# Kernel tuning notes

Hardware: AMD Instinct MI355X
Metric: run time of the kernel (lower is better)

The kernel has to match this reference:

```python
import jax, jax.numpy as jnp
import numpy as np

NUM_HEADS = 8
CH_PER_HEAD = 40
NORM_GROUPS = 32
EPS = 1e-5


def setup_inputs() -> dict:
    key = jax.random.key(0)
    ks = jax.random.split(key, 8)
    B, C, H, W = 2, 320, 48, 48
    hid = NUM_HEADS * CH_PER_HEAD  # 320
    w_std = 0.02
    return {
        "x": jax.random.normal(ks[0], (B, C, H, W), dtype=jnp.float32),
        "gamma": jnp.ones((C,), dtype=jnp.float32),
        "beta": jnp.zeros((C,), dtype=jnp.float32),
        "Wq": jax.random.normal(ks[1], (hid, C), dtype=jnp.float32) * w_std,
        "bq": jax.random.normal(ks[2], (hid,), dtype=jnp.float32) * w_std,
        "Wk": jax.random.normal(ks[3], (hid, C), dtype=jnp.float32) * w_std,
        "bk": jax.random.normal(ks[4], (hid,), dtype=jnp.float32) * w_std,
        "Wv": jax.random.normal(ks[5], (hid, C), dtype=jnp.float32) * w_std,
        "bv": jax.random.normal(ks[6], (hid,), dtype=jnp.float32) * w_std,
        "Wo": jax.random.normal(ks[7], (C, hid), dtype=jnp.float32) * w_std,
        "bo": jnp.zeros((C,), dtype=jnp.float32),
    }


def _group_norm(x, gamma, beta):
    # x: [B, C, H, W]; GroupNorm over (C//G, H, W) per group, affine per-channel.
    B, C, H, W = x.shape
    xg = x.reshape(B, NORM_GROUPS, C // NORM_GROUPS, H, W)
    mean = xg.mean(axis=(2, 3, 4), keepdims=True)
    var = xg.var(axis=(2, 3, 4), keepdims=True)
    xn = ((xg - mean) * jax.lax.rsqrt(var + EPS)).reshape(B, C, H, W)
    return xn * gamma[None, :, None, None] + beta[None, :, None, None]


def reference(x, gamma, beta, Wq, bq, Wk, bk, Wv, bv, Wo, bo):
    B, C, H, W = x.shape
    N = H * W
    h, d = NUM_HEADS, CH_PER_HEAD
    scale = d ** (-0.25)  # applied to both q and k (net 1/sqrt(d))

    xn = _group_norm(x, gamma, beta).reshape(B, C, N)  # embedding = x_n (self-attn)

    # 1x1 Conv1d == matmul over channel dim
    q = jnp.einsum('oc,bcn->bon', Wq, xn) + bq[None, :, None]
    k = jnp.einsum('oc,bcn->bon', Wk, xn) + bk[None, :, None]
    v = jnp.einsum('oc,bcn->bon', Wv, xn) + bv[None, :, None]

    # b (h d) n -> b h d n
    q = q.reshape(B, h, d, N)
    k = k.reshape(B, h, d, N)
    v = v.reshape(B, h, d, N)

    attn = jax.nn.softmax(
        jnp.einsum('bhdi,bhdj->bhij', q * scale, k * scale), axis=-1
    )  # [B, h, N, N]
    out = jnp.einsum('bhij,bhdj->bhdi', attn, v).reshape(B, h * d, N)

    out = jnp.einsum('oc,bcn->bon', Wo, out) + bo[None, :, None]
    out = out.reshape(B, C, H, W)
    return x + out  # shapes match -> residual
```

## Files before the change

kernel.cpp:

```cpp
#include <hip/hip_runtime.h>
#include <hip/hip_bf16.h>

#define C_DIM   320
#define N_SP    2304
#define NHEADS  8
#define DHEAD   40
#define GROUPS  32
#define CPG     10
#define BATCH   2
#define DPAD    64
#define VPAD    48
#define W_ELEMS (C_DIM * C_DIM)
#define NSPLIT  4
#define TILES_PER_SPLIT 9
#define PSLOTS  41

typedef __bf16 bf16x8 __attribute__((ext_vector_type(8)));
typedef __bf16 bf16x4 __attribute__((ext_vector_type(4)));
typedef __bf16 bf16x2 __attribute__((ext_vector_type(2)));
typedef float  f32x4  __attribute__((ext_vector_type(4)));

typedef const __attribute__((address_space(1))) void* gas_ptr;
typedef __attribute__((address_space(3))) void* las_ptr;

#define MFMA16(a, b, c) __builtin_amdgcn_mfma_f32_16x16x32_bf16((a), (b), (c), 0, 0, 0)

__device__ __forceinline__ void stage8(const char* gbase, char* lbase,
                                       int chunk, int lane)
{
    const int row = chunk * 8 + (lane >> 3);
    const int cs  = (lane & 7) * 16;
    __builtin_amdgcn_global_load_lds(
        (gas_ptr)(gbase + (size_t)row * (C_DIM * 2) + (cs ^ ((row & 7) << 4))),
        (las_ptr)(lbase + chunk * 1024 + lane * 16), 16, 0, 0);
}

__device__ __forceinline__ bf16x8 lds_frag(const char* lbase, int row, int cbyte)
{
    return *(const bf16x8*)(lbase + row * 128 + (cbyte ^ ((row & 7) << 4)));
}

__global__ __launch_bounds__(256) void prep_kernel(
    const float* __restrict__ x, float* __restrict__ partials,
    const float* __restrict__ Wq, const float* __restrict__ Wk,
    const float* __restrict__ Wv, const float* __restrict__ Wo,
    __bf16* __restrict__ Wqb, __bf16* __restrict__ Wkb,
    __bf16* __restrict__ Wvb, __bf16* __restrict__ Wob,
    __bf16* __restrict__ Qt, __bf16* __restrict__ Kt, __bf16* __restrict__ Vb)
{
    if (blockIdx.x < 512) {
        const int bid = blockIdx.x;
        const int bg = bid >> 3, p = bid & 7;
        const int b = bg >> 5, g = bg & 31;
        const float* xp = x + ((size_t)b * C_DIM + g * CPG) * N_SP + p * 288;
        const int tid = threadIdx.x;

        float sum = 0.f, sq = 0.f;
        #pragma unroll
        for (int c = 0; c < CPG; ++c) {
            for (int nl = tid; nl < 288; nl += 256) {
                const float v = xp[(size_t)c * N_SP + nl];
                sum += v; sq += v * v;
            }
        }
        #pragma unroll
        for (int off = 32; off; off >>= 1) {
            sum += __shfl_xor(sum, off);
            sq  += __shfl_xor(sq, off);
        }
        __shared__ float red[2][4];
        if ((tid & 63) == 0) { red[0][tid >> 6] = sum; red[1][tid >> 6] = sq; }
        __syncthreads();
        if (tid == 0) {
            partials[2 * bid]     = red[0][0] + red[0][1] + red[0][2] + red[0][3];
            partials[2 * bid + 1] = red[1][0] + red[1][1] + red[1][2] + red[1][3];
        }
    } else if (blockIdx.x < 612) {
        const int i = ((blockIdx.x - 512) * 256 + threadIdx.x) * 4;
        f32x4 a;
        bf16x4 o;
        a = *(const f32x4*)(Wq + i);
        #pragma unroll
        for (int e = 0; e < 4; ++e) o[e] = (__bf16)a[e];
        *(bf16x4*)(Wqb + i) = o;
        a = *(const f32x4*)(Wk + i);
        #pragma unroll
        for (int e = 0; e < 4; ++e) o[e] = (__bf16)a[e];
        *(bf16x4*)(Wkb + i) = o;
        a = *(const f32x4*)(Wv + i);
        #pragma unroll
        for (int e = 0; e < 4; ++e) o[e] = (__bf16)a[e];
        *(bf16x4*)(Wvb + i) = o;
        a = *(const f32x4*)(Wo + i);
        #pragma unroll
        for (int e = 0; e < 4; ++e) o[e] = (__bf16)a[e];
        *(bf16x4*)(Wob + i) = o;
    } else {
        const int t = (blockIdx.x - 612) * 256 + threadIdx.x;
        const bf16x8 z = {};
        __bf16* q = Qt + (size_t)t * DPAD + 40;
        __bf16* k = Kt + (size_t)t * DPAD + 40;
        *(bf16x8*)(q) = z; *(bf16x8*)(q + 8) = z; *(bf16x8*)(q + 16) = z;
        *(bf16x8*)(k) = z; *(bf16x8*)(k + 8) = z; *(bf16x8*)(k + 16) = z;
        const int bh = t / N_SP;
        const int rem = t - bh * N_SP;
        const int r = rem / 288, n8 = rem - r * 288;
        bf16x8 v = z;
        if (r == 0) {
            #pragma unroll
            for (int e = 0; e < 8; ++e) v[e] = (__bf16)1.0f;
        }
        *(bf16x8*)(Vb + ((size_t)bh * VPAD + 40 + r) * N_SP + n8 * 8) = v;
    }
}

__global__ __launch_bounds__(256) void gn_apply(
    const float* __restrict__ x,
    const float* __restrict__ gamma, const float* __restrict__ beta,
    const float* __restrict__ partials, __bf16* __restrict__ xn_t)
{
    const int bid = blockIdx.x;
    const int bg = bid >> 3, p = bid & 7;
    const int b = bg >> 5, g = bg & 31;
    const int c0 = g * CPG;

    float sum = 0.f, sq = 0.f;
    #pragma unroll
    for (int i = 0; i < 8; ++i) {
        sum += partials[(bg * 8 + i) * 2];
        sq  += partials[(bg * 8 + i) * 2 + 1];
    }
    const float inv_n = 1.0f / (float)(CPG * N_SP);
    const float mean = sum * inv_n;
    const float rstd = rsqrtf(sq * inv_n - mean * mean + 1e-5f);

    float ga[CPG], be[CPG];
    #pragma unroll
    for (int c = 0; c < CPG; ++c) {
        ga[c] = gamma[c0 + c] * rstd;
        be[c] = beta[c0 + c] - mean * ga[c];
    }

    const float* xp = x + ((size_t)b * C_DIM + c0) * N_SP + p * 288;
    for (int nl = threadIdx.x; nl < 288; nl += 256) {
        const int n = p * 288 + nl;
        __bf16* dst = xn_t + ((size_t)b * N_SP + n) * C_DIM + c0;
        #pragma unroll
        for (int j = 0; j < CPG / 2; ++j) {
            const float v0 = xp[(size_t)(2 * j) * N_SP + nl]     * ga[2 * j]     + be[2 * j];
            const float v1 = xp[(size_t)(2 * j + 1) * N_SP + nl] * ga[2 * j + 1] + be[2 * j + 1];
            bf16x2 t; t[0] = (__bf16)v0; t[1] = (__bf16)v1;
            *(bf16x2*)(dst + 2 * j) = t;
        }
    }
}

__global__ __launch_bounds__(256) void gemm_qkv(
    const __bf16* __restrict__ Wqb, const __bf16* __restrict__ Wkb, const __bf16* __restrict__ Wvb,
    const float* __restrict__ bq, const float* __restrict__ bk, const float* __restrict__ bv,
    const __bf16* __restrict__ Xt,
    __bf16* __restrict__ Qt, __bf16* __restrict__ Kt, __bf16* __restrict__ Vb)
{
    __shared__ __align__(16) char Ws[2][64 * 128];
    __shared__ __align__(16) char Xs[2][64 * 128];

    const int z = blockIdx.z;
    const int b = z / 3;
    const int which = z - 3 * b;
    const __bf16* W   = (which == 0) ? Wqb : (which == 1) ? Wkb : Wvb;
    const float* bias = (which == 0) ? bq : (which == 1) ? bk : bv;
    const float scale = (which == 0) ? 0.15811388300841897f
                      : (which == 1) ? 0.22811243f : 1.0f;

    const int n0 = blockIdx.x * 64, o0 = blockIdx.y * 64;
    const int tid = threadIdx.x, wave = tid >> 6, lane = tid & 63;
    const int lr = lane & 15, lk = lane >> 4;
    const int wm = wave >> 1, wn = wave & 1;

    const char* Wg = (const char*)(W + (size_t)o0 * C_DIM);
    const char* Xg = (const char*)(Xt + ((size_t)b * N_SP + n0) * C_DIM);

    auto stage = [&](int bufi, int s) {
        const int kb = s * 128;
        #pragma unroll
        for (int i = 0; i < 4; ++i) {
            const int c = wave * 4 + i;
            if (c < 8) stage8(Wg + kb, Ws[bufi], c, lane);
            else       stage8(Xg + kb, Xs[bufi], c - 8, lane);
        }
    };

    f32x4 acc[2][2] = {};

    stage(0, 0);
    __syncthreads();

    for (int s = 0; s < 5; ++s) {
        const int bufi = s & 1;
        if (s + 1 < 5) stage(bufi ^ 1, s + 1);

        const char* ws = Ws[bufi];
        const char* xs = Xs[bufi];
        __builtin_amdgcn_s_setprio(1);
        #pragma unroll
        for (int ksub = 0; ksub < 2; ++ksub) {
            const int cb = ksub * 64 + lk * 16;
            const bf16x8 a0 = lds_frag(ws, wm * 32 + lr,      cb);
            const bf16x8 a1 = lds_frag(ws, wm * 32 + 16 + lr, cb);
            const bf16x8 b0 = lds_frag(xs, wn * 32 + lr,      cb);
            const bf16x8 b1 = lds_frag(xs, wn * 32 + 16 + lr, cb);
            acc[0][0] = MFMA16(a0, b0, acc[0][0]);
            acc[0][1] = MFMA16(a0, b1, acc[0][1]);
            acc[1][0] = MFMA16(a1, b0, acc[1][0]);
            acc[1][1] = MFMA16(a1, b1, acc[1][1]);
        }
        __builtin_amdgcn_s_setprio(0);
        __syncthreads();
    }

    #pragma unroll
    for (int am = 0; am < 2; ++am) {
        #pragma unroll
        for (int rp = 0; rp < 2; ++rp) {
            const int o = o0 + wm * 32 + am * 16 + 4 * lk + 2 * rp;
            const int h = o / DHEAD, d = o - h * DHEAD;
            const int bh = b * NHEADS + h;
            const float b0_ = bias[o], b1_ = bias[o + 1];
            #pragma unroll
            for (int bn = 0; bn < 2; ++bn) {
                const int n = n0 + wn * 32 + bn * 16 + lr;
                const float v0 = (acc[am][bn][2 * rp]     + b0_) * scale;
                const float v1 = (acc[am][bn][2 * rp + 1] + b1_) * scale;
                if (which < 2) {
                    __bf16* dst = ((which == 0) ? Qt : Kt)
                                + ((size_t)bh * N_SP + n) * DPAD + d;
                    bf16x2 t; t[0] = (__bf16)v0; t[1] = (__bf16)v1;
                    *(bf16x2*)dst = t;
                } else {
                    Vb[((size_t)bh * VPAD + d)     * N_SP + n] = (__bf16)v0;
                    Vb[((size_t)bh * VPAD + d + 1) * N_SP + n] = (__bf16)v1;
                }
            }
        }
    }
}

__global__ __launch_bounds__(256) void gemm_out32(
    const __bf16* __restrict__ Wob, const float* __restrict__ bo,
    const __bf16* __restrict__ att_t,
    float* __restrict__ Y, const float* __restrict__ resid)
{
    __shared__ __align__(16) char Ws[2][32 * 128];
    __shared__ __align__(16) char Xs[2][64 * 128];

    const int b = blockIdx.z;
    const int n0 = blockIdx.x * 64, o0 = blockIdx.y * 32;
    const int tid = threadIdx.x, wave = tid >> 6, lane = tid & 63;
    const int lr = lane & 15, lk = lane >> 4;
    const int wn = wave;

    const char* Wg = (const char*)(Wob + (size_t)o0 * C_DIM);
    const char* Xg = (const char*)(att_t + ((size_t)b * N_SP + n0) * C_DIM);

    auto stage = [&](int bufi, int s) {
        const int kb = s * 128;
        #pragma unroll
        for (int i = 0; i < 3; ++i) {
            const int c = wave * 3 + i;
            if (c < 4) stage8(Wg + kb, Ws[bufi], c, lane);
            else       stage8(Xg + kb, Xs[bufi], c - 4, lane);
        }
    };

    f32x4 acc[2] = {};

    stage(0, 0);
    __syncthreads();

    for (int s = 0; s < 5; ++s) {
        const int bufi = s & 1;
        if (s + 1 < 5) stage(bufi ^ 1, s + 1);

        const char* ws = Ws[bufi];
        const char* xs = Xs[bufi];
        __builtin_amdgcn_s_setprio(1);
        #pragma unroll
        for (int ksub = 0; ksub < 2; ++ksub) {
            const int cb = ksub * 64 + lk * 16;
            const bf16x8 a0 = lds_frag(ws, lr,      cb);
            const bf16x8 a1 = lds_frag(ws, 16 + lr, cb);
            const bf16x8 b0 = lds_frag(xs, wn * 16 + lr, cb);
            acc[0] = MFMA16(a0, b0, acc[0]);
            acc[1] = MFMA16(a1, b0, acc[1]);
        }
        __builtin_amdgcn_s_setprio(0);
        __syncthreads();
    }

    const int n = n0 + wn * 16 + lr;
    #pragma unroll
    for (int am = 0; am < 2; ++am) {
        #pragma unroll
        for (int r = 0; r < 4; ++r) {
            const int o = o0 + am * 16 + 4 * lk + r;
            const size_t idx = ((size_t)b * C_DIM + o) * N_SP + n;
            Y[idx] = acc[am][r] + bo[o] + resid[idx];
        }
    }
}

__global__ __launch_bounds__(256, 4) void attn_mfma(
    const __bf16* __restrict__ Qt,
    const __bf16* __restrict__ Kt,
    const __bf16* __restrict__ Vb,
    __bf16* __restrict__ part)
{
    __shared__ __align__(16) __bf16 Ks[2][64 * DPAD];
    __shared__ __align__(16) __bf16 Vs[2][VPAD * 64];
    __shared__ __align__(16) __bf16 Ps[4][16 * 64];

    const int flat = blockIdx.x;
    const int bh = ((flat & 7) << 1) | ((flat >> 3) & 1);
    const int s  = (flat >> 4) & 3;
    const int qx = flat >> 6;
    const int tid = threadIdx.x, wave = tid >> 6, lane = tid & 63;
    const int lr = lane & 15, lk = lane >> 4;
    const int swz = (lr & 7) << 4;
    const int i0 = (qx * 4 + wave) * 32;

    const char* Kg = (const char*)(Kt + (size_t)bh * N_SP * DPAD);
    const char* Vg = (const char*)(Vb + (size_t)bh * VPAD * N_SP);

    bf16x8 qb[2][2];
    #pragma unroll
    for (int qh = 0; qh < 2; ++qh) {
        const __bf16* Qp = Qt + ((size_t)bh * N_SP + i0 + qh * 16 + lr) * DPAD + lk * 8;
        qb[qh][0] = *(const bf16x8*)(Qp);
        qb[qh][1] = *(const bf16x8*)(Qp + 32);
    }

    f32x4 O[2][3] = {};

    auto stage = [&](int bufi, int t) {
        const int j0 = t * 64;
        #pragma unroll
        for (int i2 = 0; i2 < 2; ++i2) {
            const int chunk = wave * 2 + i2;
            const int L = chunk * 1024 + lane * 16;
            const int src = L ^ (((L >> 7) & 7) << 4);
            __builtin_amdgcn_global_load_lds(
                (gas_ptr)(Kg + (size_t)j0 * 128 + src),
                (las_ptr)((char*)Ks[bufi] + chunk * 1024),
                16, 0, 0);
        }
        for (int i2 = wave; i2 < 6; i2 += 4) {
            const int row = i2 * 8 + (lane >> 3);
            const int csw = ((lane & 7) << 4) ^ ((row & 7) << 4);
            __builtin_amdgcn_global_load_lds(
                (gas_ptr)(Vg + ((size_t)row * N_SP + j0) * 2 + csw),
                (las_ptr)((char*)Vs[bufi] + i2 * 1024),
                16, 0, 0);
        }
    };

    const int t0 = s * TILES_PER_SPLIT;
    const int t1 = t0 + TILES_PER_SPLIT;

    stage(0, t0);

    for (int t = t0; t < t1; ++t) {
        const int bufi = (t - t0) & 1;
        if (t + 1 < t1) {
            stage(bufi ^ 1, t + 1);
            if (wave < 2) asm volatile("s_waitcnt vmcnt(4)" ::: "memory");
            else          asm volatile("s_waitcnt vmcnt(3)" ::: "memory");
        } else {
            asm volatile("s_waitcnt vmcnt(0)" ::: "memory");
        }
        __builtin_amdgcn_s_barrier();

        const char* ks = (const char*)Ks[bufi];
        const char* vs = (const char*)Vs[bufi];
        char* ps = (char*)Ps[wave];

        f32x4 S[2][4];
        __builtin_amdgcn_s_setprio(1);
        #pragma unroll
        for (int kt = 0; kt < 4; ++kt) {
            const int rowb = (kt * 16 + lr) * 128;
            const bf16x8 k0 = *(const bf16x8*)(ks + rowb + ((lk * 16) ^ swz));
            const bf16x8 k1 = *(const bf16x8*)(ks + rowb + ((64 + lk * 16) ^ swz));
            #pragma unroll
            for (int qh = 0; qh < 2; ++qh) {
                f32x4 zz = {};
                zz = MFMA16(k0, qb[qh][0], zz);
                S[qh][kt] = MFMA16(k1, qb[qh][1], zz);
            }
        }
        __builtin_amdgcn_s_setprio(0);

        bf16x8 va[2][3];
        #pragma unroll
        for (int hh = 0; hh < 2; ++hh)
            #pragma unroll
            for (int dt = 0; dt < 3; ++dt)
                va[hh][dt] = *(const bf16x8*)(vs + (dt * 16 + lr) * 128
                                              + ((hh * 64 + lk * 16) ^ swz));

        #pragma unroll
        for (int qh = 0; qh < 2; ++qh) {
            #pragma unroll
            for (int kt = 0; kt < 4; ++kt) {
                bf16x4 w;
                #pragma unroll
                for (int r = 0; r < 4; ++r)
                    w[r] = (__bf16)exp2f(S[qh][kt][r]);
                *(bf16x4*)(ps + lr * 128 + ((kt * 32 + lk * 8) ^ swz)) = w;
            }
            __builtin_amdgcn_s_setprio(1);
            #pragma unroll
            for (int hh = 0; hh < 2; ++hh) {
                const bf16x8 pb = *(const bf16x8*)(ps + lr * 128 + ((hh * 64 + lk * 16) ^ swz));
                #pragma unroll
                for (int dt = 0; dt < 3; ++dt)
                    O[qh][dt] = MFMA16(va[hh][dt], pb, O[qh][dt]);
            }
            __builtin_amdgcn_s_setprio(0);
        }

        __builtin_amdgcn_s_barrier();
    }

    #pragma unroll
    for (int qh = 0; qh < 2; ++qh) {
        __bf16* pq = part + ((size_t)(s * 16 + bh) * PSLOTS) * N_SP + (i0 + qh * 16 + lr);
        #pragma unroll
        for (int dt = 0; dt < 3; ++dt) {
            #pragma unroll
            for (int r = 0; r < 4; ++r) {
                const int d = dt * 16 + 4 * lk + r;
                if (d < 40) pq[(size_t)d * N_SP] = (__bf16)O[qh][dt][r];
            }
        }
        if (lk == 2) pq[(size_t)40 * N_SP] = (__bf16)O[qh][2][0];
    }
}

__global__ __launch_bounds__(256) void attn_combine(
    const __bf16* __restrict__ part, __bf16* __restrict__ att_t)
{
    const int q = blockIdx.x * 256 + threadIdx.x;
    const int bh = blockIdx.y, b = bh >> 3, h = bh & 7;

    const __bf16* p[NSPLIT];
    float l = 0.f;
    #pragma unroll
    for (int s = 0; s < NSPLIT; ++s) {
        p[s] = part + ((size_t)(s * 16 + bh) * PSLOTS) * N_SP + q;
        l += (float)p[s][(size_t)40 * N_SP];
    }
    const float inv = 1.0f / l;

    __bf16* op = att_t + ((size_t)b * N_SP + q) * C_DIM + h * DHEAD;
    #pragma unroll
    for (int d2 = 0; d2 < DHEAD / 2; ++d2) {
        float a0 = 0.f, a1 = 0.f;
        #pragma unroll
        for (int s = 0; s < NSPLIT; ++s) {
            a0 += (float)p[s][(size_t)(2 * d2) * N_SP];
            a1 += (float)p[s][(size_t)(2 * d2 + 1) * N_SP];
        }
        bf16x2 t;
        t[0] = (__bf16)(a0 * inv);
        t[1] = (__bf16)(a1 * inv);
        *(bf16x2*)(op + 2 * d2) = t;
    }
}

extern "C" void kernel_launch(void* const* d_in, const int* in_sizes, int n_in,
                              void* d_out, int out_size, void* d_ws, size_t ws_size,
                              hipStream_t stream) {
    const float* x     = (const float*)d_in[0];
    const float* gamma = (const float*)d_in[1];
    const float* beta  = (const float*)d_in[2];
    const float* Wq    = (const float*)d_in[3];
    const float* bq    = (const float*)d_in[4];
    const float* Wk    = (const float*)d_in[5];
    const float* bk    = (const float*)d_in[6];
    const float* Wv    = (const float*)d_in[7];
    const float* bv    = (const float*)d_in[8];
    const float* Wo    = (const float*)d_in[9];
    const float* bo    = (const float*)d_in[10];

    float* out = (float*)d_out;

    const size_t S_NC  = (size_t)BATCH * N_SP * C_DIM;
    const size_t S_QK  = (size_t)BATCH * NHEADS * N_SP * DPAD;
    const size_t S_V   = (size_t)BATCH * NHEADS * VPAD * N_SP;

    __bf16* xn_t  = (__bf16*)d_ws;
    __bf16* Qt    = xn_t + S_NC;
    __bf16* Kt    = Qt + S_QK;
    __bf16* Vb    = Kt + S_QK;
    __bf16* att_t = Vb + S_V;
    __bf16* Wqb   = att_t + S_NC;
    __bf16* Wkb   = Wqb + W_ELEMS;
    __bf16* Wvb   = Wkb + W_ELEMS;
    __bf16* Wob   = Wvb + W_ELEMS;
    float* partials = (float*)(Wob + W_ELEMS);
    __bf16* part    = (__bf16*)(partials + 1024);

    prep_kernel<<<756, 256, 0, stream>>>(
        x, partials, Wq, Wk, Wv, Wo, Wqb, Wkb, Wvb, Wob, Qt, Kt, Vb);

    gn_apply<<<512, 256, 0, stream>>>(x, gamma, beta, partials, xn_t);

    gemm_qkv<<<dim3(N_SP / 64, C_DIM / 64, 3 * BATCH), 256, 0, stream>>>(
        Wqb, Wkb, Wvb, bq, bk, bv, xn_t, Qt, Kt, Vb);

    attn_mfma<<<dim3(18 * 16 * NSPLIT), 256, 0, stream>>>(Qt, Kt, Vb, part);

    attn_combine<<<dim3(N_SP / 256, BATCH * NHEADS), 256, 0, stream>>>(part, att_t);

    gemm_out32<<<dim3(N_SP / 64, C_DIM / 32, BATCH), 256, 0, stream>>>(
        Wob, bo, att_t, out, x);
}
```

Baseline: 78.72 us.

## Reduce attention KV splits to three and unroll double-buffer loop by two

```diff
diff --git a/kernel.cpp b/kernel.cpp
--- a/kernel.cpp
+++ b/kernel.cpp
@@ -11,8 +11,8 @@
 #define DPAD    64
 #define VPAD    48
 #define W_ELEMS (C_DIM * C_DIM)
-#define NSPLIT  4
-#define TILES_PER_SPLIT 9
+#define NSPLIT  3
+#define TILES_PER_SPLIT 12
 #define PSLOTS  41
 
 typedef __bf16 bf16x8 __attribute__((ext_vector_type(8)));
@@ -321,8 +321,9 @@
 
     const int flat = blockIdx.x;
     const int bh = ((flat & 7) << 1) | ((flat >> 3) & 1);
-    const int s  = (flat >> 4) & 3;
-    const int qx = flat >> 6;
+    const int rest = flat >> 4;
+    const int qx = rest / 3;
+    const int s  = rest - 3 * qx;
     const int tid = threadIdx.x, wave = tid >> 6, lane = tid & 63;
     const int lr = lane & 15, lk = lane >> 4;
     const int swz = (lr & 7) << 4;
@@ -341,7 +342,7 @@
 
     f32x4 O[2][3] = {};
 
-    auto stage = [&](int bufi, int t) {
+    auto stage = [&](char* kd, char* vd, int t) {
         const int j0 = t * 64;
         #pragma unroll
         for (int i2 = 0; i2 < 2; ++i2) {
@@ -350,37 +351,18 @@
             const int src = L ^ (((L >> 7) & 7) << 4);
             __builtin_amdgcn_global_load_lds(
                 (gas_ptr)(Kg + (size_t)j0 * 128 + src),
-                (las_ptr)((char*)Ks[bufi] + chunk * 1024),
-                16, 0, 0);
+                (las_ptr)(kd + chunk * 1024), 16, 0, 0);
         }
         for (int i2 = wave; i2 < 6; i2 += 4) {
             const int row = i2 * 8 + (lane >> 3);
             const int csw = ((lane & 7) << 4) ^ ((row & 7) << 4);
             __builtin_amdgcn_global_load_lds(
                 (gas_ptr)(Vg + ((size_t)row * N_SP + j0) * 2 + csw),
-                (las_ptr)((char*)Vs[bufi] + i2 * 1024),
-                16, 0, 0);
+                (las_ptr)(vd + i2 * 1024), 16, 0, 0);
         }
     };
 
-    const int t0 = s * TILES_PER_SPLIT;
-    const int t1 = t0 + TILES_PER_SPLIT;
-
-    stage(0, t0);
-
-    for (int t = t0; t < t1; ++t) {
-        const int bufi = (t - t0) & 1;
-        if (t + 1 < t1) {
-            stage(bufi ^ 1, t + 1);
-            if (wave < 2) asm volatile("s_waitcnt vmcnt(4)" ::: "memory");
-            else          asm volatile("s_waitcnt vmcnt(3)" ::: "memory");
-        } else {
-            asm volatile("s_waitcnt vmcnt(0)" ::: "memory");
-        }
-        __builtin_amdgcn_s_barrier();
-
-        const char* ks = (const char*)Ks[bufi];
-        const char* vs = (const char*)Vs[bufi];
+    auto compute = [&](const char* ks, const char* vs) {
         char* ps = (char*)Ps[wave];
 
         f32x4 S[2][4];
@@ -427,8 +409,34 @@
             }
             __builtin_amdgcn_s_setprio(0);
         }
-
-        __builtin_amdgcn_s_barrier();
+    };
+
+    const int t0 = s * TILES_PER_SPLIT;
+
+    stage((char*)Ks[0], (char*)Vs[0], t0);
+
+    #pragma unroll 1
+    for (int tt = 0; tt < TILES_PER_SPLIT; tt += 2) {
+        {
+            stage((char*)Ks[1], (char*)Vs[1], t0 + tt + 1);
+            if (wave < 2) asm volatile("s_waitcnt vmcnt(4)" ::: "memory");
+            else          asm volatile("s_waitcnt vmcnt(3)" ::: "memory");
+            __builtin_amdgcn_s_barrier();
+            compute((const char*)Ks[0], (const char*)Vs[0]);
+            __builtin_amdgcn_s_barrier();
+        }
+        {
+            if (tt + 2 < TILES_PER_SPLIT) {
+                stage((char*)Ks[0], (char*)Vs[0], t0 + tt + 2);
+                if (wave < 2) asm volatile("s_waitcnt vmcnt(4)" ::: "memory");
+                else          asm volatile("s_waitcnt vmcnt(3)" ::: "memory");
+            } else {
+                asm volatile("s_waitcnt vmcnt(0)" ::: "memory");
+            }
+            __builtin_amdgcn_s_barrier();
+            compute((const char*)Ks[1], (const char*)Vs[1]);
+            __builtin_amdgcn_s_barrier();
+        }
     }
 
     #pragma unroll
```

Result: no change. 78.12 us (-0.8%).
